# Performance work log

Hardware: AMD Instinct MI355X
Metric: run time of the kernel (lower is better)

Reference implementation:

```python
import jax, jax.numpy as jnp
import numpy as np

D_MODEL = 1024
N_HEADS = 16
D_K = D_MODEL // N_HEADS
D_FF = 4096
B, S = 2, 2048
LN_EPS = 1e-5
NEG_INF = -1e30  # finite stand-in for -inf; first (all-masked) row is overwritten by zeros anyway


def layer_norm(x, g, b):
    mu = jnp.mean(x, axis=-1, keepdims=True)
    var = jnp.mean(jnp.square(x - mu), axis=-1, keepdims=True)
    return (x - mu) * jax.lax.rsqrt(var + LN_EPS) * g + b


def setup_inputs() -> dict:
    key = jax.random.key(0)
    ks = jax.random.split(key, 16)
    sd = 0.02
    inp = {
        "query": jax.random.normal(ks[0], (B, S, D_MODEL), jnp.float32),
        "key": jax.random.normal(ks[1], (B, S, D_MODEL), jnp.float32),
        "values": jax.random.normal(ks[2], (B, S, D_MODEL), jnp.float32),
        "Wq": jax.random.normal(ks[3], (D_MODEL, D_MODEL), jnp.float32) * sd,
        "bq": jnp.zeros((D_MODEL,), jnp.float32),
        "Wk": jax.random.normal(ks[4], (D_MODEL, D_MODEL), jnp.float32) * sd,
        "bk": jnp.zeros((D_MODEL,), jnp.float32),
        "Wv": jax.random.normal(ks[5], (D_MODEL, D_MODEL), jnp.float32) * sd,
        "bv": jnp.zeros((D_MODEL,), jnp.float32),
        "Wo": jax.random.normal(ks[6], (D_MODEL, D_MODEL), jnp.float32) * sd,
        "bo": jnp.zeros((D_MODEL,), jnp.float32),
        "ln1_g": jnp.ones((D_MODEL,), jnp.float32),
        "ln1_b": jnp.zeros((D_MODEL,), jnp.float32),
        "W1": jax.random.normal(ks[7], (D_MODEL, D_FF), jnp.float32) * sd,
        "b1": jnp.zeros((D_FF,), jnp.float32),
        "W2": jax.random.normal(ks[8], (D_FF, D_MODEL), jnp.float32) * sd,
        "b2": jnp.zeros((D_MODEL,), jnp.float32),
        "ln2_g": jnp.ones((D_MODEL,), jnp.float32),
        "ln2_b": jnp.zeros((D_MODEL,), jnp.float32),
        "mask": 0,
    }
    return inp


def reference(query, key, values, Wq, bq, Wk, bk, Wv, bv, Wo, bo,
              ln1_g, ln1_b, W1, b1, W2, b2, ln2_g, ln2_b, mask):
    b, s, d = query.shape
    # projections -> [B, H, S, d_k]
    q = (query @ Wq + bq).reshape(b, s, N_HEADS, D_K).transpose(0, 2, 1, 3)
    k = (key @ Wk + bk).reshape(b, s, N_HEADS, D_K).transpose(0, 2, 1, 3)
    v = (values @ Wv + bv).reshape(b, s, N_HEADS, D_K).transpose(0, 2, 1, 3)
    # scores [B, H, S, S]
    scores = jnp.einsum("bhqd,bhkd->bhqk", q, k) / jnp.sqrt(jnp.float32(D_K))
    # torch: triu(ones, k=mask)==0 -> allowed iff j < i + mask
    i = jnp.arange(s)[:, None]
    j = jnp.arange(s)[None, :]
    allowed = j < (i + mask)
    scores = jnp.where(allowed, scores, NEG_INF)
    attn = jax.nn.softmax(scores, axis=-1)
    if mask == 0:
        # zero-pad trick: first query row (fully masked) is replaced by zeros
        attn = attn.at[:, :, 0, :].set(0.0)
    ctx = jnp.einsum("bhqk,bhkd->bhqd", attn, v)
    ctx = ctx.transpose(0, 2, 1, 3).reshape(b, s, d)
    attn_out = ctx @ Wo + bo
    x = layer_norm(query + attn_out, ln1_g, ln1_b)
    ffn = jax.nn.relu(x @ W1 + b1) @ W2 + b2
    out = layer_norm(x + ffn, ln2_g, ln2_b)
    return out
```

## Files before the change

### kernel.cpp

```cpp
#include <hip/hip_runtime.h>


typedef __attribute__((ext_vector_type(8))) __bf16 bf16x8;
typedef __attribute__((ext_vector_type(4))) float f32x4;
typedef __attribute__((ext_vector_type(8))) short s16x8;

struct alignas(8)  S4 { short x, y, z, w; };
struct alignas(16) F4 { float x, y, z, w; };

static __device__ __forceinline__ short f2bf(float f) {
  unsigned u = __float_as_uint(f);
  u += 0x7fff + ((u >> 16) & 1);
  return (short)(u >> 16);
}

static __device__ __forceinline__ short f2bf_fast(float f) {
  union { __bf16 h; short s; } u;
  u.h = (__bf16)f;
  return u.s;
}

#if __has_builtin(__builtin_amdgcn_exp2f)
#define EXP2F(x) __builtin_amdgcn_exp2f(x)
#else
#define EXP2F(x) exp2f(x)
#endif
#define SM_SCALE 0.18033688011112042f

static __device__ __forceinline__ void store_out(float* p, float v) { *p = v; }
static __device__ __forceinline__ void store_out(short* p, float v) { *p = f2bf(v); }

#define GLL16(g, l)                                                         \
  __builtin_amdgcn_global_load_lds(                                         \
      (__attribute__((address_space(1))) void*)(g),                         \
      (__attribute__((address_space(3))) void*)(l), 16, 0, 0)

__global__ __launch_bounds__(256) void cvt_bf16_kernel(
    const float* __restrict__ i0, const float* __restrict__ i1,
    const float* __restrict__ i2, short* __restrict__ o0,
    short* __restrict__ o1, short* __restrict__ o2) {
  int z = blockIdx.y;
  const float* in = z == 0 ? i0 : (z == 1 ? i1 : i2);
  short* out = z == 0 ? o0 : (z == 1 ? o1 : o2);
  int i = (blockIdx.x * 256 + threadIdx.x) * 4;
  F4 v = *(const F4*)(in + i);
  S4 o = { f2bf(v.x), f2bf(v.y), f2bf(v.z), f2bf(v.w) };
  *(S4*)(out + i) = o;
}

__global__ __launch_bounds__(256) void transpose_cvt_kernel(
    const float* __restrict__ Wq, const float* __restrict__ Wk,
    const float* __restrict__ Wv, const float* __restrict__ Wo,
    const float* __restrict__ W1, const float* __restrict__ W2,
    short* __restrict__ Wqt, short* __restrict__ Wkt,
    short* __restrict__ Wvt, short* __restrict__ Wot,
    short* __restrict__ W1t, short* __restrict__ W2t) {
  __shared__ float tile[64][65];
  int bid = blockIdx.x;
  const float* W; short* Wt; int K, N, kx, ny;
  if (bid < 1024) {
    int w = bid >> 8, t = bid & 255;
    W = w == 0 ? Wq : (w == 1 ? Wk : (w == 2 ? Wv : Wo));
    Wt = w == 0 ? Wqt : (w == 1 ? Wkt : (w == 2 ? Wvt : Wot));
    K = 1024; N = 1024; kx = t & 15; ny = t >> 4;
  } else if (bid < 2048) {
    int t = bid - 1024;
    W = W1; Wt = W1t; K = 1024; N = 4096; kx = t & 15; ny = t >> 4;
  } else {
    int t = bid - 2048;
    W = W2; Wt = W2t; K = 4096; N = 1024; kx = t & 63; ny = t >> 6;
  }
  int k0 = kx * 64, n0 = ny * 64;
  int tid = threadIdx.x;
  int rr = tid >> 4, cc = (tid & 15) * 4;
#pragma unroll
  for (int p = 0; p < 4; ++p) {
    int row = p * 16 + rr;
    F4 v = *(const F4*)&W[(long)(k0 + row) * N + n0 + cc];
    tile[row][cc] = v.x; tile[row][cc + 1] = v.y;
    tile[row][cc + 2] = v.z; tile[row][cc + 3] = v.w;
  }
  __syncthreads();
#pragma unroll
  for (int p = 0; p < 4; ++p) {
    int rn = p * 16 + rr;
    S4 o = { f2bf(tile[cc + 0][rn]), f2bf(tile[cc + 1][rn]),
             f2bf(tile[cc + 2][rn]), f2bf(tile[cc + 3][rn]) };
    *(S4*)&Wt[(long)(n0 + rn) * K + k0 + cc] = o;
  }
}

template <int NF, int OUT_MODE, bool RELU, typename OT>
__device__ __forceinline__ void gemm256_core(
    const short* __restrict__ A, const short* __restrict__ Bt,
    const float* __restrict__ bias, OT* __restrict__ out,
    int N, int K, int kBeg, int kEnd, int m0, int n0) {
  constexpr int BN = NF * 64;
  constexpr int LB = BN / 64;
  __shared__ __align__(16) short sA[2][256 * 64];
  __shared__ __align__(16) short sB[2][BN * 64];
  int tid = threadIdx.x;
  int lane = tid & 63, wave = tid >> 6;
  int col = lane & 15, quad = lane >> 4;
  int wm = (wave >> 2) * 128;
  int wn = (wave & 3) * (NF * 16);

  f32x4 acc[8][NF] = {};

  const int NT = (kEnd - kBeg) >> 6;
  const int t0 = kBeg >> 6;

  auto stageA = [&](int buf, int kt) {
#pragma unroll
    for (int j = 0; j < 4; ++j) {
      int idx = j * 512 + tid;
      int row = idx >> 3, cp = idx & 7;
      int c = cp ^ (row & 7);
      GLL16(A + (long)(m0 + row) * K + kt * 64 + c * 8,
            &sA[buf][(j * 512 + (wave << 6)) * 8]);
    }
  };
  auto stageB = [&](int buf, int kt) {
#pragma unroll
    for (int j = 0; j < LB; ++j) {
      int idx = j * 512 + tid;
      int row = idx >> 3, cp = idx & 7;
      int c = cp ^ (row & 7);
      GLL16(Bt + (long)(n0 + row) * K + kt * 64 + c * 8,
            &sB[buf][(j * 512 + (wave << 6)) * 8]);
    }
  };

  stageA(0, t0);     stageB(0, t0);
  stageA(1, t0 + 1); stageB(1, t0 + 1);
  if constexpr (NF == 4) asm volatile("s_waitcnt vmcnt(8)" ::: "memory");
  else                   asm volatile("s_waitcnt vmcnt(6)" ::: "memory");
  __builtin_amdgcn_sched_barrier(0);
  __builtin_amdgcn_s_barrier();

  for (int t = 0; t < NT; ++t) {
    int cur = t & 1;
    bool pf = (t + 2 < NT);
    bf16x8 bf[NF][2], af[2][2];

#pragma unroll
    for (int n = 0; n < NF; ++n) {
      int rb = wn + n * 16 + col;
#pragma unroll
      for (int kk = 0; kk < 2; ++kk) {
        int ca = kk * 4 + quad;
        bf[n][kk] = *(const bf16x8*)&sB[cur][rb * 64 + ((ca ^ (rb & 7)) << 3)];
      }
    }
#pragma unroll
    for (int i = 0; i < 2; ++i) {
      int ra = wm + i * 16 + col;
#pragma unroll
      for (int kk = 0; kk < 2; ++kk) {
        int ca = kk * 4 + quad;
        af[i][kk] = *(const bf16x8*)&sA[cur][ra * 64 + ((ca ^ (ra & 7)) << 3)];
      }
    }
    asm volatile("s_waitcnt lgkmcnt(0)" ::: "memory");
    __builtin_amdgcn_sched_barrier(0);
    __builtin_amdgcn_s_setprio(1);
#pragma unroll
    for (int i = 0; i < 2; ++i)
#pragma unroll
      for (int n = 0; n < NF; ++n)
#pragma unroll
        for (int kk = 0; kk < 2; ++kk)
          acc[i][n] = __builtin_amdgcn_mfma_f32_16x16x32_bf16(
              af[i][kk], bf[n][kk], acc[i][n], 0, 0, 0);
    __builtin_amdgcn_s_setprio(0);
    __builtin_amdgcn_s_barrier();
    __builtin_amdgcn_sched_barrier(0);

    if (pf) stageB(cur, t0 + t + 2);
#pragma unroll
    for (int i = 0; i < 2; ++i) {
      int ra = wm + (2 + i) * 16 + col;
#pragma unroll
      for (int kk = 0; kk < 2; ++kk) {
        int ca = kk * 4 + quad;
        af[i][kk] = *(const bf16x8*)&sA[cur][ra * 64 + ((ca ^ (ra & 7)) << 3)];
      }
    }
    __builtin_amdgcn_s_setprio(1);
#pragma unroll
    for (int i = 0; i < 2; ++i)
#pragma unroll
      for (int n = 0; n < NF; ++n)
#pragma unroll
        for (int kk = 0; kk < 2; ++kk)
          acc[2 + i][n] = __builtin_amdgcn_mfma_f32_16x16x32_bf16(
              af[i][kk], bf[n][kk], acc[2 + i][n], 0, 0, 0);
    __builtin_amdgcn_s_setprio(0);
    __builtin_amdgcn_s_barrier();

#pragma unroll
    for (int i = 0; i < 2; ++i) {
      int ra = wm + (4 + i) * 16 + col;
#pragma unroll
      for (int kk = 0; kk < 2; ++kk) {
        int ca = kk * 4 + quad;
        af[i][kk] = *(const bf16x8*)&sA[cur][ra * 64 + ((ca ^ (ra & 7)) << 3)];
      }
    }
    __builtin_amdgcn_s_setprio(1);
#pragma unroll
    for (int i = 0; i < 2; ++i)
#pragma unroll
      for (int n = 0; n < NF; ++n)
#pragma unroll
        for (int kk = 0; kk < 2; ++kk)
          acc[4 + i][n] = __builtin_amdgcn_mfma_f32_16x16x32_bf16(
              af[i][kk], bf[n][kk], acc[4 + i][n], 0, 0, 0);
    __builtin_amdgcn_s_setprio(0);
    __builtin_amdgcn_s_barrier();

#pragma unroll
    for (int i = 0; i < 2; ++i) {
      int ra = wm + (6 + i) * 16 + col;
#pragma unroll
      for (int kk = 0; kk < 2; ++kk) {
        int ca = kk * 4 + quad;
        af[i][kk] = *(const bf16x8*)&sA[cur][ra * 64 + ((ca ^ (ra & 7)) << 3)];
      }
    }
    asm volatile("s_waitcnt lgkmcnt(0)" ::: "memory");
    __builtin_amdgcn_sched_barrier(0);
    __builtin_amdgcn_s_barrier();
    __builtin_amdgcn_sched_barrier(0);
    if (pf) stageA(cur, t0 + t + 2);
    __builtin_amdgcn_s_setprio(1);
#pragma unroll
    for (int i = 0; i < 2; ++i)
#pragma unroll
      for (int n = 0; n < NF; ++n)
#pragma unroll
        for (int kk = 0; kk < 2; ++kk)
          acc[6 + i][n] = __builtin_amdgcn_mfma_f32_16x16x32_bf16(
              af[i][kk], bf[n][kk], acc[6 + i][n], 0, 0, 0);
    __builtin_amdgcn_s_setprio(0);
    if (pf) {
      if constexpr (NF == 4) asm volatile("s_waitcnt vmcnt(8)" ::: "memory");
      else                   asm volatile("s_waitcnt vmcnt(6)" ::: "memory");
    } else {
      asm volatile("s_waitcnt vmcnt(0)" ::: "memory");
    }
    __builtin_amdgcn_sched_barrier(0);
    __builtin_amdgcn_s_barrier();
  }

#pragma unroll
  for (int m = 0; m < 8; ++m) {
#pragma unroll
    for (int n = 0; n < NF; ++n) {
      int Cc = n0 + wn + n * 16 + col;
      float bv = bias ? bias[Cc] : 0.f;
#pragma unroll
      for (int r = 0; r < 4; ++r) {
        int R = m0 + wm + m * 16 + quad * 4 + r;
        float v = acc[m][n][r] + bv;
        if (RELU) v = v > 0.f ? v : 0.f;
        if (OUT_MODE == 0) {
          store_out(&out[(long)R * N + Cc], v);
        } else {
          int bb = R >> 11, s = R & 2047, h = Cc >> 6, d = Cc & 63;
          store_out(&out[((long)((bb * 16 + h) * 2048 + s) << 6) + d], v);
        }
      }
    }
  }
}

__device__ __forceinline__ void gsp128_core(
    const short* __restrict__ A, const short* __restrict__ Bt,
    const float* __restrict__ bias, float* __restrict__ out,
    int N, int K, int kBeg, int kEnd, int m0, int n0) {
  __shared__ __align__(16) short sA[2][256 * 64];
  __shared__ __align__(16) short sB[2][128 * 64];
  int tid = threadIdx.x;
  int lane = tid & 63, wave = tid >> 6;
  int col = lane & 15, quad = lane >> 4;
  int wm = (wave >> 1) * 64;
  int wn = (wave & 1) * 64;

  f32x4 acc[4][4] = {};
  const int NT = (kEnd - kBeg) >> 6;
  const int t0 = kBeg >> 6;

  auto stageA = [&](int buf, int kt) {
#pragma unroll
    for (int j = 0; j < 4; ++j) {
      int idx = j * 512 + tid;
      int row = idx >> 3, cp = idx & 7;
      int c = cp ^ (row & 7);
      GLL16(A + (long)(m0 + row) * K + kt * 64 + c * 8,
            &sA[buf][(j * 512 + (wave << 6)) * 8]);
    }
  };
  auto stageB = [&](int buf, int kt) {
#pragma unroll
    for (int j = 0; j < 2; ++j) {
      int idx = j * 512 + tid;
      int row = idx >> 3, cp = idx & 7;
      int c = cp ^ (row & 7);
      GLL16(Bt + (long)(n0 + row) * K + kt * 64 + c * 8,
            &sB[buf][(j * 512 + (wave << 6)) * 8]);
    }
  };

  stageA(0, t0);     stageB(0, t0);
  stageA(1, t0 + 1); stageB(1, t0 + 1);
  asm volatile("s_waitcnt vmcnt(6)" ::: "memory");
  __builtin_amdgcn_s_barrier();

  for (int t = 0; t < NT; ++t) {
    int cur = t & 1;
    bool pf = (t + 2 < NT);
    bf16x8 bf[4][2], af[4][2];

#pragma unroll
    for (int n = 0; n < 4; ++n) {
      int rb = wn + n * 16 + col;
#pragma unroll
      for (int kk = 0; kk < 2; ++kk) {
        int ca = kk * 4 + quad;
        bf[n][kk] = *(const bf16x8*)&sB[cur][rb * 64 + ((ca ^ (rb & 7)) << 3)];
      }
    }
#pragma unroll
    for (int m = 0; m < 4; ++m) {
      int ra = wm + m * 16 + col;
#pragma unroll
      for (int kk = 0; kk < 2; ++kk) {
        int ca = kk * 4 + quad;
        af[m][kk] = *(const bf16x8*)&sA[cur][ra * 64 + ((ca ^ (ra & 7)) << 3)];
      }
    }
    asm volatile("s_waitcnt lgkmcnt(0)" ::: "memory");
    __builtin_amdgcn_s_barrier();
    __builtin_amdgcn_sched_barrier(0);
    if (pf) { stageA(cur, t0 + t + 2); stageB(cur, t0 + t + 2); }
    __builtin_amdgcn_s_setprio(1);
#pragma unroll
    for (int m = 0; m < 4; ++m)
#pragma unroll
      for (int n = 0; n < 4; ++n)
#pragma unroll
        for (int kk = 0; kk < 2; ++kk)
          acc[m][n] = __builtin_amdgcn_mfma_f32_16x16x32_bf16(
              af[m][kk], bf[n][kk], acc[m][n], 0, 0, 0);
    __builtin_amdgcn_s_setprio(0);
    if (pf) asm volatile("s_waitcnt vmcnt(6)" ::: "memory");
    else    asm volatile("s_waitcnt vmcnt(0)" ::: "memory");
    __builtin_amdgcn_s_barrier();
  }

#pragma unroll
  for (int m = 0; m < 4; ++m) {
#pragma unroll
    for (int n = 0; n < 4; ++n) {
      int Cc = n0 + wn + n * 16 + col;
      float bv = bias ? bias[Cc] : 0.f;
#pragma unroll
      for (int r = 0; r < 4; ++r) {
        int R = m0 + wm + m * 16 + quad * 4 + r;
        out[(long)R * N + Cc] = acc[m][n][r] + bv;
      }
    }
  }
}

__global__ __launch_bounds__(512) void g256_ffn1(
    const short* __restrict__ A, const short* __restrict__ Bt,
    const float* __restrict__ bias, short* __restrict__ out) {
  gemm256_core<4, 0, true, short>(A, Bt, bias, out, 4096, 1024, 0, 1024,
                                  blockIdx.x * 256, blockIdx.y * 256);
}

__global__ __launch_bounds__(512) void g256_qkv(
    const short* __restrict__ Aq, const short* __restrict__ Ak,
    const short* __restrict__ Av, const short* __restrict__ Btq,
    const short* __restrict__ Btk, const short* __restrict__ Btv,
    const float* __restrict__ bq, const float* __restrict__ bk,
    const float* __restrict__ bv, short* __restrict__ Qp,
    short* __restrict__ Kp, short* __restrict__ Vp) {
  int z = blockIdx.z;
  const short* A = z == 0 ? Aq : (z == 1 ? Ak : Av);
  const short* Bt = z == 0 ? Btq : (z == 1 ? Btk : Btv);
  const float* bias = z == 0 ? bq : (z == 1 ? bk : bv);
  short* out = z == 0 ? Qp : (z == 1 ? Kp : Vp);
  gemm256_core<4, 1, false, short>(A, Bt, bias, out, 1024, 1024, 0, 1024,
                                   blockIdx.x * 256, blockIdx.y * 256);
}

__global__ __launch_bounds__(512) void gsp_wo(
    const short* __restrict__ A, const short* __restrict__ Bt,
    const float* __restrict__ bias, float* __restrict__ p0,
    float* __restrict__ p1) {
  int z = blockIdx.z;
  float* out = z == 0 ? p0 : p1;
  const float* b = z == 0 ? bias : nullptr;
  gsp128_core(A, Bt, b, out, 1024, 1024, z * 512, z * 512 + 512,
              blockIdx.x * 256, blockIdx.y * 128);
}

__global__ __launch_bounds__(512) void gsp_ffn2(
    const short* __restrict__ A, const short* __restrict__ Bt,
    const float* __restrict__ bias, float* __restrict__ p0,
    float* __restrict__ p1) {
  int z = blockIdx.z;
  float* out = z == 0 ? p0 : p1;
  const float* b = z == 0 ? bias : nullptr;
  gsp128_core(A, Bt, b, out, 1024, 4096, z * 2048, z * 2048 + 2048,
              blockIdx.x * 256, blockIdx.y * 128);
}

__global__ __launch_bounds__(256) void attn_kernel(
    const short* __restrict__ Q, const short* __restrict__ K,
    const short* __restrict__ V, const int* __restrict__ maskp,
    short* __restrict__ ctx) {
  __shared__ __align__(16) short sK[2][64 * 64];
  __shared__ __align__(16) int   sVt[2][64 * 32];
  __shared__ __align__(16) short sP[4 * 16 * 64];
  int tid = threadIdx.x, wave = tid >> 6;
  int lane = tid & 63;
  int col = lane & 15, quad = lane >> 4;
  int bh = blockIdx.x, pair = blockIdx.y;
  int maskv = maskp[0];
  const long base = (long)bh * (2048 * 64);
  int b = bh >> 4, h = bh & 15;

  int kp = tid & 31, dg = tid >> 5, d0v = dg * 8;

  for (int pass = 0; pass < 2; ++pass) {
    int qt = pass ? (31 - pair) : pair;
    int i0 = qt * 64 + wave * 16;

    long jmax = (long)qt * 64 + 63 + maskv - 1;
    int tot = (jmax < 0) ? 0 : (int)(jmax >> 6) + 1;
    if (tot > 32) tot = 32;

    bf16x8 aQ[2];
#pragma unroll
    for (int kk = 0; kk < 2; ++kk)
      aQ[kk] = *(const bf16x8*)&Q[base + (long)(i0 + col) * 64 + kk * 32 + quad * 8];

    f32x4 o[4] = {};
    float lsum[4] = { 0.f, 0.f, 0.f, 0.f };

    if (tot > 0) {
#pragma unroll
      for (int j = 0; j < 2; ++j) {
        int idx = j * 256 + tid;
        int row = idx >> 3, cp = idx & 7;
        int c = cp ^ (row & 7);
        GLL16(K + base + (long)row * 64 + c * 8,
              &sK[0][(j * 256 + (wave << 6)) * 8]);
      }
      {
        s16x8 u0 = *(const s16x8*)&V[base + (long)(2 * kp) * 64 + d0v];
        s16x8 u1 = *(const s16x8*)&V[base + (long)(2 * kp + 1) * 64 + d0v];
#pragma unroll
        for (int j = 0; j < 8; ++j) {
          int d = d0v + j;
          int w = ((int)(unsigned short)u1[j] << 16) | (unsigned short)u0[j];
          sVt[0][d * 32 + ((((kp >> 2) ^ (d & 7)) << 2) | (kp & 3))] = w;
        }
      }
    }
    __syncthreads();

    for (int kt = 0; kt < tot; ++kt) {
      int cur = kt & 1, nxt = cur ^ 1;
      bool pf = (kt + 1 < tot);

      s16x8 u0, u1;
      if (pf) {
#pragma unroll
        for (int j = 0; j < 2; ++j) {
          int idx = j * 256 + tid;
          int row = idx >> 3, cp = idx & 7;
          int c = cp ^ (row & 7);
          GLL16(K + base + (long)((kt + 1) * 64 + row) * 64 + c * 8,
                &sK[nxt][(j * 256 + (wave << 6)) * 8]);
        }
        u0 = *(const s16x8*)&V[base + (long)((kt + 1) * 64 + 2 * kp) * 64 + d0v];
        u1 = *(const s16x8*)&V[base + (long)((kt + 1) * 64 + 2 * kp + 1) * 64 + d0v];
      }

      f32x4 sc[4] = {};
      __builtin_amdgcn_s_setprio(1);
#pragma unroll
      for (int kk = 0; kk < 2; ++kk) {
        int ca = kk * 4 + quad;
#pragma unroll
        for (int nt = 0; nt < 4; ++nt) {
          int rk = nt * 16 + col;
          bf16x8 bK = *(const bf16x8*)&sK[cur][rk * 64 + ((ca ^ (rk & 7)) << 3)];
          sc[nt] = __builtin_amdgcn_mfma_f32_16x16x32_bf16(aQ[kk], bK, sc[nt], 0, 0, 0);
        }
      }
      __builtin_amdgcn_s_setprio(0);

      bool interior = (kt * 64 + 63) < (i0 + maskv);
      if (interior) {
#pragma unroll
        for (int r = 0; r < 4; ++r) {
          int qr = quad * 4 + r;
#pragma unroll
          for (int nt = 0; nt < 4; ++nt) {
            float p = EXP2F(sc[nt][r] * SM_SCALE);
            lsum[r] += p;
            int k8 = nt * 2 + (col >> 3);
            sP[wave * 1024 + qr * 64 + (((k8 ^ (qr & 7)) << 3) | (col & 7))] =
                f2bf_fast(p);
          }
        }
      } else {
#pragma unroll
        for (int r = 0; r < 4; ++r) {
          int i = i0 + quad * 4 + r;
          int qr = quad * 4 + r;
#pragma unroll
          for (int nt = 0; nt < 4; ++nt) {
            int j = kt * 64 + nt * 16 + col;
            float p = (j < i + maskv) ? EXP2F(sc[nt][r] * SM_SCALE) : 0.f;
            lsum[r] += p;
            int k8 = nt * 2 + (col >> 3);
            sP[wave * 1024 + qr * 64 + (((k8 ^ (qr & 7)) << 3) | (col & 7))] =
                f2bf_fast(p);
          }
        }
      }

      __builtin_amdgcn_s_setprio(1);
#pragma unroll
      for (int kk = 0; kk < 2; ++kk) {
        int ca = kk * 4 + quad;
        bf16x8 aP = *(const bf16x8*)&sP[wave * 1024 + col * 64 + ((ca ^ (col & 7)) << 3)];
#pragma unroll
        for (int dt = 0; dt < 4; ++dt) {
          int d = dt * 16 + col;
          bf16x8 bV = *(const bf16x8*)((const short*)sVt[cur] + d * 64 + ((ca ^ (d & 7)) << 3));
          o[dt] = __builtin_amdgcn_mfma_f32_16x16x32_bf16(aP, bV, o[dt], 0, 0, 0);
        }
      }
      __builtin_amdgcn_s_setprio(0);

      if (pf) {
#pragma unroll
        for (int j = 0; j < 8; ++j) {
          int d = d0v + j;
          int w = ((int)(unsigned short)u1[j] << 16) | (unsigned short)u0[j];
          sVt[nxt][d * 32 + ((((kp >> 2) ^ (d & 7)) << 2) | (kp & 3))] = w;
        }
      }
      __syncthreads();
    }

#pragma unroll
    for (int r = 0; r < 4; ++r)
#pragma unroll
      for (int off = 1; off < 16; off <<= 1)
        lsum[r] += __shfl_xor(lsum[r], off);

#pragma unroll
    for (int r = 0; r < 4; ++r) {
      int i = i0 + quad * 4 + r;
      float inv = (lsum[r] > 0.f) ? 1.f / lsum[r] : 0.f;
      if (maskv == 0 && i == 0) inv = 0.f;
#pragma unroll
      for (int dt = 0; dt < 4; ++dt)
        ctx[(long)(b * 2048 + i) * 1024 + h * 64 + dt * 16 + col] =
            f2bf(o[dt][r] * inv);
    }
  }
}

__global__ __launch_bounds__(256) void ln_comb_kernel(
    const float* __restrict__ p0, const float* __restrict__ p1,
    const float* __restrict__ res, const float* __restrict__ g,
    const float* __restrict__ b, float* __restrict__ outf,
    short* __restrict__ outb) {
  int r = blockIdx.x, tid = threadIdx.x;
  int lane = tid & 63, wave = tid >> 6;
  long off0 = (long)r * 1024;
  F4 a = ((const F4*)(p0 + off0))[tid];
  F4 c = ((const F4*)(p1 + off0))[tid];
  F4 d = ((const F4*)(res + off0))[tid];
  F4 v = { a.x + c.x + d.x, a.y + c.y + d.y, a.z + c.z + d.z, a.w + c.w + d.w };
  float s = v.x + v.y + v.z + v.w;
  float sq = v.x * v.x + v.y * v.y + v.z * v.z + v.w * v.w;
#pragma unroll
  for (int off = 1; off < 64; off <<= 1) {
    s += __shfl_xor(s, off);
    sq += __shfl_xor(sq, off);
  }
  __shared__ float rs[4], rq[4];
  if (lane == 0) { rs[wave] = s; rq[wave] = sq; }
  __syncthreads();
  s = rs[0] + rs[1] + rs[2] + rs[3];
  sq = rq[0] + rq[1] + rq[2] + rq[3];
  float mu = s * (1.0f / 1024.0f);
  float var = sq * (1.0f / 1024.0f) - mu * mu;
  float rstd = rsqrtf(var + 1e-5f);
  F4 gv = ((const F4*)g)[tid], bv = ((const F4*)b)[tid];
  F4 o;
  o.x = (v.x - mu) * rstd * gv.x + bv.x;
  o.y = (v.y - mu) * rstd * gv.y + bv.y;
  o.z = (v.z - mu) * rstd * gv.z + bv.z;
  o.w = (v.w - mu) * rstd * gv.w + bv.w;
  ((F4*)(outf + off0))[tid] = o;
  if (outb) {
    S4 ob = { f2bf(o.x), f2bf(o.y), f2bf(o.z), f2bf(o.w) };
    ((S4*)(outb + off0))[tid] = ob;
  }
}

extern "C" void kernel_launch(void* const* d_in, const int* in_sizes, int n_in,
                              void* d_out, int out_size, void* d_ws, size_t ws_size,
                              hipStream_t stream) {
  const float* query  = (const float*)d_in[0];
  const float* keyi   = (const float*)d_in[1];
  const float* values = (const float*)d_in[2];
  const float* Wq = (const float*)d_in[3];
  const float* bq = (const float*)d_in[4];
  const float* Wk = (const float*)d_in[5];
  const float* bk = (const float*)d_in[6];
  const float* Wv = (const float*)d_in[7];
  const float* bv = (const float*)d_in[8];
  const float* Wo = (const float*)d_in[9];
  const float* bo = (const float*)d_in[10];
  const float* ln1_g = (const float*)d_in[11];
  const float* ln1_b = (const float*)d_in[12];
  const float* W1 = (const float*)d_in[13];
  const float* b1 = (const float*)d_in[14];
  const float* W2 = (const float*)d_in[15];
  const float* b2 = (const float*)d_in[16];
  const float* ln2_g = (const float*)d_in[17];
  const float* ln2_b = (const float*)d_in[18];
  const int*   maskp = (const int*)d_in[19];
  float* out = (float*)d_out;

  char* ws = (char*)d_ws;
  const size_t MB = 1u << 20;
  short* q_bf = (short*)(ws + 0);
  short* k_bf = (short*)(ws + 8 * MB);
  short* v_bf = (short*)(ws + 16 * MB);
  short* ctx  = (short*)(ws + 24 * MB);
  short* Qp   = (short*)(ws + 32 * MB);
  short* Kp   = (short*)(ws + 40 * MB);
  short* Vp   = (short*)(ws + 48 * MB);
  short* Wqt  = (short*)(ws + 56 * MB);
  short* Wkt  = (short*)(ws + 58 * MB);
  short* Wvt  = (short*)(ws + 60 * MB);
  short* Wot  = (short*)(ws + 62 * MB);
  short* W1t  = (short*)(ws + 64 * MB);
  short* W2t  = (short*)(ws + 72 * MB);
  short* hbuf = (short*)(ws + 80 * MB);
  float* pWo0 = (float*)(ws + 0);
  float* pWo1 = (float*)(ws + 32 * MB);
  float* x_f32 = (float*)(ws + 16 * MB);
  short* x_bf  = (short*)(ws + 48 * MB);
  float* pF0 = (float*)(ws + 0);
  float* pF1 = (float*)(ws + 32 * MB);

  cvt_bf16_kernel<<<dim3(4096, 3), 256, 0, stream>>>(query, keyi, values,
                                                     q_bf, k_bf, v_bf);
  transpose_cvt_kernel<<<3072, 256, 0, stream>>>(Wq, Wk, Wv, Wo, W1, W2,
                                                 Wqt, Wkt, Wvt, Wot, W1t, W2t);
  g256_qkv<<<dim3(16, 4, 3), 512, 0, stream>>>(q_bf, k_bf, v_bf,
                                               Wqt, Wkt, Wvt,
                                               bq, bk, bv, Qp, Kp, Vp);
  attn_kernel<<<dim3(32, 16), 256, 0, stream>>>(Qp, Kp, Vp, maskp, ctx);
  gsp_wo<<<dim3(16, 8, 2), 512, 0, stream>>>(ctx, Wot, bo, pWo0, pWo1);
  ln_comb_kernel<<<4096, 256, 0, stream>>>(pWo0, pWo1, query, ln1_g, ln1_b,
                                           x_f32, x_bf);
  g256_ffn1<<<dim3(16, 16), 512, 0, stream>>>(x_bf, W1t, b1, hbuf);
  gsp_ffn2<<<dim3(16, 8, 2), 512, 0, stream>>>(hbuf, W2t, b2, pF0, pF1);
  ln_comb_kernel<<<4096, 256, 0, stream>>>(pF0, pF1, x_f32, ln2_g, ln2_b,
                                           out, nullptr);

  (void)in_sizes; (void)n_in; (void)out_size; (void)ws_size;
}
```

Measured before the change: 369.9 us.

## Enlarge attention query tile to 128 rows with split-K waves and LDS reduction

```diff
diff --git a/kernel.cpp b/kernel.cpp
--- a/kernel.cpp
+++ b/kernel.cpp
@@ -419,55 +419,58 @@
               blockIdx.x * 256, blockIdx.y * 128);
 }
 
-__global__ __launch_bounds__(256) void attn_kernel(
+__global__ __launch_bounds__(512) void attn_kernel(
     const short* __restrict__ Q, const short* __restrict__ K,
     const short* __restrict__ V, const int* __restrict__ maskp,
     short* __restrict__ ctx) {
   __shared__ __align__(16) short sK[2][64 * 64];
   __shared__ __align__(16) int   sVt[2][64 * 32];
-  __shared__ __align__(16) short sP[4 * 16 * 64];
+  __shared__ __align__(16) short sP[8 * 32 * 64];
+  __shared__ float sLred[128];
   int tid = threadIdx.x, wave = tid >> 6;
   int lane = tid & 63;
   int col = lane & 15, quad = lane >> 4;
+  int g = wave >> 2, wlow = wave & 3;
   int bh = blockIdx.x, pair = blockIdx.y;
   int maskv = maskp[0];
   const long base = (long)bh * (2048 * 64);
   int b = bh >> 4, h = bh & 15;
 
-  int kp = tid & 31, dg = tid >> 5, d0v = dg * 8;
+  int kp = tid & 31, dg = tid >> 5, d0v = dg * 4;
 
   for (int pass = 0; pass < 2; ++pass) {
-    int qt = pass ? (31 - pair) : pair;
-    int i0 = qt * 64 + wave * 16;
-
-    long jmax = (long)qt * 64 + 63 + maskv - 1;
+    int qt = pass ? (15 - pair) : pair;
+    int iq0 = qt * 128 + wlow * 32;
+
+    long jmax = (long)qt * 128 + 127 + maskv - 1;
     int tot = (jmax < 0) ? 0 : (int)(jmax >> 6) + 1;
     if (tot > 32) tot = 32;
 
-    bf16x8 aQ[2];
-#pragma unroll
-    for (int kk = 0; kk < 2; ++kk)
-      aQ[kk] = *(const bf16x8*)&Q[base + (long)(i0 + col) * 64 + kk * 32 + quad * 8];
-
-    f32x4 o[4] = {};
-    float lsum[4] = { 0.f, 0.f, 0.f, 0.f };
+    bf16x8 aQ[2][2];
+#pragma unroll
+    for (int mt = 0; mt < 2; ++mt)
+#pragma unroll
+      for (int kk = 0; kk < 2; ++kk)
+        aQ[mt][kk] = *(const bf16x8*)&Q[base +
+            (long)(iq0 + mt * 16 + col) * 64 + kk * 32 + quad * 8];
+
+    f32x4 o[2][4] = {};
+    float lsum[2][4] = {};
 
     if (tot > 0) {
-#pragma unroll
-      for (int j = 0; j < 2; ++j) {
-        int idx = j * 256 + tid;
-        int row = idx >> 3, cp = idx & 7;
+      {
+        int row = tid >> 3, cp = tid & 7;
         int c = cp ^ (row & 7);
-        GLL16(K + base + (long)row * 64 + c * 8,
-              &sK[0][(j * 256 + (wave << 6)) * 8]);
+        GLL16(K + base + (long)row * 64 + c * 8, &sK[0][(wave << 6) * 8]);
       }
       {
-        s16x8 u0 = *(const s16x8*)&V[base + (long)(2 * kp) * 64 + d0v];
-        s16x8 u1 = *(const s16x8*)&V[base + (long)(2 * kp + 1) * 64 + d0v];
-#pragma unroll
-        for (int j = 0; j < 8; ++j) {
+        union { S4 v; short s[4]; } u0, u1;
+        u0.v = *(const S4*)&V[base + (long)(2 * kp) * 64 + d0v];
+        u1.v = *(const S4*)&V[base + (long)(2 * kp + 1) * 64 + d0v];
+#pragma unroll
+        for (int j = 0; j < 4; ++j) {
           int d = d0v + j;
-          int w = ((int)(unsigned short)u1[j] << 16) | (unsigned short)u0[j];
+          int w = ((int)(unsigned short)u1.s[j] << 16) | (unsigned short)u0.s[j];
           sVt[0][d * 32 + ((((kp >> 2) ^ (d & 7)) << 2) | (kp & 3))] = w;
         }
       }
@@ -478,84 +481,96 @@
       int cur = kt & 1, nxt = cur ^ 1;
       bool pf = (kt + 1 < tot);
 
-      s16x8 u0, u1;
+      union { S4 v; short s[4]; } u0, u1;
       if (pf) {
-#pragma unroll
-        for (int j = 0; j < 2; ++j) {
-          int idx = j * 256 + tid;
-          int row = idx >> 3, cp = idx & 7;
-          int c = cp ^ (row & 7);
-          GLL16(K + base + (long)((kt + 1) * 64 + row) * 64 + c * 8,
-                &sK[nxt][(j * 256 + (wave << 6)) * 8]);
-        }
-        u0 = *(const s16x8*)&V[base + (long)((kt + 1) * 64 + 2 * kp) * 64 + d0v];
-        u1 = *(const s16x8*)&V[base + (long)((kt + 1) * 64 + 2 * kp + 1) * 64 + d0v];
-      }
-
-      f32x4 sc[4] = {};
+        int row = tid >> 3, cp = tid & 7;
+        int c = cp ^ (row & 7);
+        GLL16(K + base + (long)((kt + 1) * 64 + row) * 64 + c * 8,
+              &sK[nxt][(wave << 6) * 8]);
+        u0.v = *(const S4*)&V[base + (long)((kt + 1) * 64 + 2 * kp) * 64 + d0v];
+        u1.v = *(const S4*)&V[base + (long)((kt + 1) * 64 + 2 * kp + 1) * 64 + d0v];
+      }
+
+      f32x4 sc[2][2] = {};
       __builtin_amdgcn_s_setprio(1);
 #pragma unroll
       for (int kk = 0; kk < 2; ++kk) {
         int ca = kk * 4 + quad;
 #pragma unroll
-        for (int nt = 0; nt < 4; ++nt) {
-          int rk = nt * 16 + col;
+        for (int nt = 0; nt < 2; ++nt) {
+          int rk = (2 * g + nt) * 16 + col;
           bf16x8 bK = *(const bf16x8*)&sK[cur][rk * 64 + ((ca ^ (rk & 7)) << 3)];
-          sc[nt] = __builtin_amdgcn_mfma_f32_16x16x32_bf16(aQ[kk], bK, sc[nt], 0, 0, 0);
+#pragma unroll
+          for (int mt = 0; mt < 2; ++mt)
+            sc[mt][nt] = __builtin_amdgcn_mfma_f32_16x16x32_bf16(
+                aQ[mt][kk], bK, sc[mt][nt], 0, 0, 0);
         }
       }
       __builtin_amdgcn_s_setprio(0);
 
-      bool interior = (kt * 64 + 63) < (i0 + maskv);
+      bool interior = (kt * 64 + g * 32 + 31) < (iq0 + maskv);
       if (interior) {
 #pragma unroll
-        for (int r = 0; r < 4; ++r) {
-          int qr = quad * 4 + r;
-#pragma unroll
-          for (int nt = 0; nt < 4; ++nt) {
-            float p = EXP2F(sc[nt][r] * SM_SCALE);
-            lsum[r] += p;
-            int k8 = nt * 2 + (col >> 3);
-            sP[wave * 1024 + qr * 64 + (((k8 ^ (qr & 7)) << 3) | (col & 7))] =
-                f2bf_fast(p);
+        for (int mt = 0; mt < 2; ++mt)
+#pragma unroll
+          for (int r = 0; r < 4; ++r) {
+            int qr = mt * 16 + quad * 4 + r;
+#pragma unroll
+            for (int nt = 0; nt < 2; ++nt) {
+              float p = EXP2F(sc[mt][nt][r] * SM_SCALE);
+              lsum[mt][r] += p;
+              int k8 = 4 * g + nt * 2 + (col >> 3);
+              sP[wave * 2048 + qr * 64 + (((k8 ^ (qr & 7)) << 3) | (col & 7))] =
+                  f2bf_fast(p);
+            }
           }
-        }
       } else {
 #pragma unroll
-        for (int r = 0; r < 4; ++r) {
-          int i = i0 + quad * 4 + r;
-          int qr = quad * 4 + r;
-#pragma unroll
-          for (int nt = 0; nt < 4; ++nt) {
-            int j = kt * 64 + nt * 16 + col;
-            float p = (j < i + maskv) ? EXP2F(sc[nt][r] * SM_SCALE) : 0.f;
-            lsum[r] += p;
-            int k8 = nt * 2 + (col >> 3);
-            sP[wave * 1024 + qr * 64 + (((k8 ^ (qr & 7)) << 3) | (col & 7))] =
-                f2bf_fast(p);
+        for (int mt = 0; mt < 2; ++mt)
+#pragma unroll
+          for (int r = 0; r < 4; ++r) {
+            int i = iq0 + mt * 16 + quad * 4 + r;
+            int qr = mt * 16 + quad * 4 + r;
+#pragma unroll
+            for (int nt = 0; nt < 2; ++nt) {
+              int j = kt * 64 + (2 * g + nt) * 16 + col;
+              float p = (j < i + maskv) ? EXP2F(sc[mt][nt][r] * SM_SCALE) : 0.f;
+              lsum[mt][r] += p;
+              int k8 = 4 * g + nt * 2 + (col >> 3);
+              sP[wave * 2048 + qr * 64 + (((k8 ^ (qr & 7)) << 3) | (col & 7))] =
+                  f2bf_fast(p);
+            }
           }
-        }
-      }
-
-      __builtin_amdgcn_s_setprio(1);
-#pragma unroll
-      for (int kk = 0; kk < 2; ++kk) {
-        int ca = kk * 4 + quad;
-        bf16x8 aP = *(const bf16x8*)&sP[wave * 1024 + col * 64 + ((ca ^ (col & 7)) << 3)];
+      }
+
+      {
+        int ca = 4 * g + quad;
+        bf16x8 bV[4];
 #pragma unroll
         for (int dt = 0; dt < 4; ++dt) {
           int d = dt * 16 + col;
-          bf16x8 bV = *(const bf16x8*)((const short*)sVt[cur] + d * 64 + ((ca ^ (d & 7)) << 3));
-          o[dt] = __builtin_amdgcn_mfma_f32_16x16x32_bf16(aP, bV, o[dt], 0, 0, 0);
+          bV[dt] = *(const bf16x8*)((const short*)sVt[cur] + d * 64 +
+                                    ((ca ^ (d & 7)) << 3));
         }
-      }
-      __builtin_amdgcn_s_setprio(0);
+        __builtin_amdgcn_s_setprio(1);
+#pragma unroll
+        for (int mt = 0; mt < 2; ++mt) {
+          int rp = mt * 16 + col;
+          bf16x8 aP = *(const bf16x8*)&sP[wave * 2048 + rp * 64 +
+                                          ((ca ^ (rp & 7)) << 3)];
+#pragma unroll
+          for (int dt = 0; dt < 4; ++dt)
+            o[mt][dt] = __builtin_amdgcn_mfma_f32_16x16x32_bf16(
+                aP, bV[dt], o[mt][dt], 0, 0, 0);
+        }
+        __builtin_amdgcn_s_setprio(0);
+      }
 
       if (pf) {
 #pragma unroll
-        for (int j = 0; j < 8; ++j) {
+        for (int j = 0; j < 4; ++j) {
           int d = d0v + j;
-          int w = ((int)(unsigned short)u1[j] << 16) | (unsigned short)u0[j];
+          int w = ((int)(unsigned short)u1.s[j] << 16) | (unsigned short)u0.s[j];
           sVt[nxt][d * 32 + ((((kp >> 2) ^ (d & 7)) << 2) | (kp & 3))] = w;
         }
       }
@@ -563,21 +578,56 @@
     }
 
 #pragma unroll
-    for (int r = 0; r < 4; ++r)
-#pragma unroll
-      for (int off = 1; off < 16; off <<= 1)
-        lsum[r] += __shfl_xor(lsum[r], off);
-
-#pragma unroll
-    for (int r = 0; r < 4; ++r) {
-      int i = i0 + quad * 4 + r;
-      float inv = (lsum[r] > 0.f) ? 1.f / lsum[r] : 0.f;
-      if (maskv == 0 && i == 0) inv = 0.f;
-#pragma unroll
-      for (int dt = 0; dt < 4; ++dt)
-        ctx[(long)(b * 2048 + i) * 1024 + h * 64 + dt * 16 + col] =
-            f2bf(o[dt][r] * inv);
-    }
+    for (int mt = 0; mt < 2; ++mt)
+#pragma unroll
+      for (int r = 0; r < 4; ++r)
+#pragma unroll
+        for (int off = 1; off < 16; off <<= 1)
+          lsum[mt][r] += __shfl_xor(lsum[mt][r], off);
+
+    float* od = (float*)sP;
+    int slot = wlow * 64 + lane;
+    if (g == 1) {
+#pragma unroll
+      for (int mt = 0; mt < 2; ++mt)
+#pragma unroll
+        for (int dt = 0; dt < 4; ++dt)
+          *(f32x4*)&od[slot * 32 + (((mt * 4 + dt) ^ (lane & 7)) << 2)] =
+              o[mt][dt];
+      if (col == 0) {
+#pragma unroll
+        for (int mt = 0; mt < 2; ++mt)
+#pragma unroll
+          for (int r = 0; r < 4; ++r)
+            sLred[wlow * 32 + mt * 16 + quad * 4 + r] = lsum[mt][r];
+      }
+    }
+    __syncthreads();
+    if (g == 0) {
+#pragma unroll
+      for (int mt = 0; mt < 2; ++mt) {
+#pragma unroll
+        for (int dt = 0; dt < 4; ++dt) {
+          f32x4 t = *(const f32x4*)&od[slot * 32 +
+                                       (((mt * 4 + dt) ^ (lane & 7)) << 2)];
+          o[mt][dt] += t;
+        }
+      }
+#pragma unroll
+      for (int mt = 0; mt < 2; ++mt)
+#pragma unroll
+        for (int r = 0; r < 4; ++r) {
+          float ls = lsum[mt][r] + sLred[wlow * 32 + mt * 16 + quad * 4 + r];
+          int i = iq0 + mt * 16 + quad * 4 + r;
+          float inv = (ls > 0.f) ? 1.f / ls : 0.f;
+          if (maskv == 0 && i == 0) inv = 0.f;
+#pragma unroll
+          for (int dt = 0; dt < 4; ++dt)
+            ctx[(long)(b * 2048 + i) * 1024 + h * 64 + dt * 16 + col] =
+                f2bf(o[mt][dt][r] * inv);
+        }
+    }
+    __syncthreads();
   }
 }
 
@@ -676,7 +726,7 @@
   g256_qkv<<<dim3(16, 4, 3), 512, 0, stream>>>(q_bf, k_bf, v_bf,
                                                Wqt, Wkt, Wvt,
                                                bq, bk, bv, Qp, Kp, Vp);
-  attn_kernel<<<dim3(32, 16), 256, 0, stream>>>(Qp, Kp, Vp, maskp, ctx);
+  attn_kernel<<<dim3(32, 8), 512, 0, stream>>>(Qp, Kp, Vp, maskp, ctx);
   gsp_wo<<<dim3(16, 8, 2), 512, 0, stream>>>(ctx, Wot, bo, pWo0, pWo1);
   ln_comb_kernel<<<4096, 256, 0, stream>>>(pWo0, pWo1, query, ln1_g, ln1_b,
                                            x_f32, x_bf);
```

Measured after the change: 382.7 us. +3.4%, slower.
